# Kernel optimization log

Hardware: AMD Instinct MI355X
Metric: run time of the kernel (lower is better)

The kernel has to match this reference:

```python
import jax, jax.numpy as jnp
import numpy as np

D_MODEL = 1024
NUM_HEADS = 16
D_K = 1024
D_V = 1024
D_IN = 1024
THETA = 10000.0
B, S = 2, 2048


def setup_inputs() -> dict:
    key = jax.random.key(0)
    k1, k2, k3, k4, k5 = jax.random.split(key, 5)
    std_qkv = (2.0 / (D_IN + D_K)) ** 0.5
    std_o = (2.0 / (D_V + D_MODEL)) ** 0.5
    x = jax.random.normal(k1, (B, S, D_IN), jnp.float32)
    wq = jax.random.normal(k2, (D_IN, D_K), jnp.float32) * std_qkv
    wk = jax.random.normal(k3, (D_IN, D_K), jnp.float32) * std_qkv
    wv = jax.random.normal(k4, (D_IN, D_V), jnp.float32) * std_qkv
    wo = jax.random.normal(k5, (D_V, D_MODEL), jnp.float32) * std_o
    return {"x": x, "wq": wq, "wk": wk, "wv": wv, "wo": wo}


def _rope(t, theta):
    # t: (H, B, S, hd) -- interleaved-pair RoPE, angles pos * theta^(-2i/hd)
    hd = t.shape[-1]
    inv_freq = 1.0 / (theta ** (jnp.arange(0, hd, 2, dtype=jnp.float32) / hd))  # (hd/2,)
    pos = jnp.arange(t.shape[-2], dtype=jnp.float32)
    ang = pos[:, None] * inv_freq[None, :]                                       # (S, hd/2)
    cos, sin = jnp.cos(ang), jnp.sin(ang)
    tp = t.reshape(t.shape[:-1] + (hd // 2, 2))
    t0, t1 = tp[..., 0], tp[..., 1]
    out = jnp.stack([t0 * cos - t1 * sin, t0 * sin + t1 * cos], axis=-1)
    return out.reshape(t.shape)


def reference(x, wq, wk, wv, wo):
    b, s, _ = x.shape
    hd = D_K // NUM_HEADS
    hdv = D_V // NUM_HEADS
    # fused QKV proj (math identical to concat-then-matmul)
    q = jnp.einsum('bsd,de->bse', x, wq).reshape(b, s, NUM_HEADS, hd).transpose(2, 0, 1, 3)
    k = jnp.einsum('bsd,de->bse', x, wk).reshape(b, s, NUM_HEADS, hd).transpose(2, 0, 1, 3)
    v = jnp.einsum('bsd,de->bse', x, wv).reshape(b, s, NUM_HEADS, hdv).transpose(2, 0, 1, 3)
    q = _rope(q, THETA)
    k = _rope(k, THETA)
    scale = 1.0 / jnp.sqrt(jnp.asarray(hd, jnp.float32))
    scores = jnp.einsum('hbqd,hbkd->hbqk', q, k) * scale                 # (H,B,S,S)
    causal = jnp.tril(jnp.ones((s, s), dtype=bool))
    scores = jnp.where(causal, scores, -jnp.inf)
    attn = jax.nn.softmax(scores, axis=-1)
    o = jnp.einsum('hbqk,hbkd->hbqd', attn, v)                            # (H,B,S,hdv)
    o = o.transpose(1, 2, 0, 3).reshape(b, s, D_V)                        # merge heads (outer)
    return jnp.einsum('bsd,de->bse', o, wo)
```

## Files before the change

### kernel.cpp

```cpp
#include <hip/hip_runtime.h>
#include <stdint.h>

typedef __attribute__((ext_vector_type(8))) short short8;
typedef __attribute__((ext_vector_type(4))) float f32x4;
typedef __attribute__((ext_vector_type(4))) unsigned short ushort4v;
typedef __attribute__((ext_vector_type(2))) unsigned int uint2v;

static __device__ __forceinline__ unsigned short f2b(float f) {
  union { float f; unsigned int u; } v; v.f = f;
  unsigned int r = v.u + 0x7FFFu + ((v.u >> 16) & 1u);
  return (unsigned short)(r >> 16);
}

static __device__ __forceinline__ float exp2fast(float x) {
#if __has_builtin(__builtin_amdgcn_exp2f)
  return __builtin_amdgcn_exp2f(x);
#else
  return exp2f(x);
#endif
}

static __device__ __forceinline__ unsigned int cvtpk(float lo, float hi) {
  unsigned int r;
  asm("v_cvt_pk_bf16_f32 %0, %1, %2" : "=v"(r) : "v"(lo), "v"(hi));
  return r;
}

static __device__ __forceinline__ float xor16max(float x) {
#if __has_builtin(__builtin_amdgcn_permlane16_swap)
  unsigned u = __float_as_uint(x);
  uint2v r = __builtin_amdgcn_permlane16_swap(u, u, false, false);
  return fmaxf(__uint_as_float(r[0]), __uint_as_float(r[1]));
#else
  return fmaxf(x, __shfl_xor(x, 16));
#endif
}
static __device__ __forceinline__ float xor32max(float x) {
#if __has_builtin(__builtin_amdgcn_permlane32_swap)
  unsigned u = __float_as_uint(x);
  uint2v r = __builtin_amdgcn_permlane32_swap(u, u, false, false);
  return fmaxf(__uint_as_float(r[0]), __uint_as_float(r[1]));
#else
  return fmaxf(x, __shfl_xor(x, 32));
#endif
}
static __device__ __forceinline__ float xor16add(float x) {
#if __has_builtin(__builtin_amdgcn_permlane16_swap)
  unsigned u = __float_as_uint(x);
  uint2v r = __builtin_amdgcn_permlane16_swap(u, u, false, false);
  return __uint_as_float(r[0]) + __uint_as_float(r[1]);
#else
  return x + __shfl_xor(x, 16);
#endif
}
static __device__ __forceinline__ float xor32add(float x) {
#if __has_builtin(__builtin_amdgcn_permlane32_swap)
  unsigned u = __float_as_uint(x);
  uint2v r = __builtin_amdgcn_permlane32_swap(u, u, false, false);
  return __uint_as_float(r[0]) + __uint_as_float(r[1]);
#else
  return x + __shfl_xor(x, 32);
#endif
}

static __device__ __forceinline__ void gload16(const void* g, void* l) {
  __builtin_amdgcn_global_load_lds(
      (const __attribute__((address_space(1))) unsigned int*)g,
      (__attribute__((address_space(3))) unsigned int*)l, 16, 0, 0);
}


__global__ __launch_bounds__(256) void prep_kernel(
    const float* __restrict__ x, const float* __restrict__ wq,
    const float* __restrict__ wk, const float* __restrict__ wv,
    const float* __restrict__ wo, unsigned short* __restrict__ xb,
    unsigned short* __restrict__ wT, float* __restrict__ ct,
    float* __restrict__ st) {
  __shared__ float t[32][33];
  const int bid = blockIdx.x, tid = threadIdx.x;
  if (bid < 4096) {
    int i = (bid * 256 + tid) * 4;
    float4 v = *(const float4*)(x + i);
    ushort4v o = { f2b(v.x), f2b(v.y), f2b(v.z), f2b(v.w) };
    *(ushort4v*)(xb + i) = o;
  } else if (bid < 8192) {
    int tt = bid - 4096;
    int z = tt >> 10, xy = tt & 1023;
    const float* src = (z == 0) ? wq : (z == 1) ? wk : (z == 2) ? wv : wo;
    unsigned short* dst = wT + (size_t)z * 1048576;
    int tx = tid & 31, ty = tid >> 5;
    int n0 = (xy & 31) * 32, k0 = (xy >> 5) * 32;
#pragma unroll
    for (int i = 0; i < 4; ++i) {
      int r = ty + i * 8;
      t[r][tx] = src[(size_t)(k0 + r) * 1024 + n0 + tx];
    }
    __syncthreads();
#pragma unroll
    for (int i = 0; i < 4; ++i) {
      int r = ty + i * 8;
      dst[(size_t)(n0 + r) * 1024 + k0 + tx] = f2b(t[tx][r]);
    }
  } else {
    int i = (bid - 8192) * 256 + tid;
    int s = i >> 5, p = i & 31;
    float ang = (float)s * powf(10000.0f, -(float)(2 * p) / 64.0f);
    ct[i] = cosf(ang);
    st[i] = sinf(ang);
  }
}


__global__ __launch_bounds__(256) void gemm_kernel(
    const unsigned short* __restrict__ A, const unsigned short* __restrict__ WT,
    unsigned short* __restrict__ Qb, unsigned short* __restrict__ Kb,
    unsigned short* __restrict__ VTb,
    const float* __restrict__ ctab, const float* __restrict__ stab) {
  __shared__ unsigned short As[2][128 * 32];
  __shared__ unsigned short Bs[2][128 * 32];
  const int tid = threadIdx.x;
  const int w = tid >> 6, lane = tid & 63;
  const int m0 = blockIdx.x * 128, n0 = blockIdx.y * 128;
  const int mode = blockIdx.z;
  const unsigned short* Bt = WT + (size_t)mode * 1048576;
  const int wr = w >> 1, wc = w & 1;
  const int srow = lane >> 2, scol = lane & 3;
  f32x4 acc[4][4] = {};
  for (int k0 = 0; k0 < 1024; k0 += 64) {
#pragma unroll
    for (int p = 0; p < 2; ++p)
#pragma unroll
      for (int c = 0; c < 2; ++c) {
        int chunk = w * 2 + c;
        gload16(A + (size_t)(m0 + chunk * 16 + srow) * 1024 + k0 + p * 32 + scol * 8,
                (char*)As[p] + chunk * 1024);
        gload16(Bt + (size_t)(n0 + chunk * 16 + srow) * 1024 + k0 + p * 32 + scol * 8,
                (char*)Bs[p] + chunk * 1024);
      }
    __syncthreads();
#pragma unroll
    for (int p = 0; p < 2; ++p) {
      short8 af[4], bf[4];
#pragma unroll
      for (int i = 0; i < 4; ++i) {
        af[i] = *(const short8*)((const char*)As[p] +
                ((wr * 64 + i * 16 + (lane & 15)) * 64 + (lane >> 4) * 16));
        bf[i] = *(const short8*)((const char*)Bs[p] +
                ((wc * 64 + i * 16 + (lane & 15)) * 64 + (lane >> 4) * 16));
      }
#pragma unroll
      for (int i = 0; i < 4; ++i)
#pragma unroll
        for (int j = 0; j < 4; ++j)
          acc[i][j] = __builtin_amdgcn_mfma_f32_16x16x32_bf16(af[i], bf[j], acc[i][j], 0, 0, 0);
    }
    __syncthreads();
  }

  if (mode < 2) {
    unsigned short* dst = mode ? Kb : Qb;
    const float qscale = mode ? 1.0f : 0.125f * 1.44269504088896f;
#pragma unroll
    for (int i = 0; i < 4; ++i) {
#pragma unroll
      for (int j = 0; j < 4; ++j) {
        int n = n0 + wc * 64 + j * 16 + (lane & 15);
        int h = n >> 6, d = n & 63;
        int pairIdx = d >> 1;
        bool even = (n & 1) == 0;
#pragma unroll
        for (int r = 0; r < 4; ++r) {
          int m = m0 + wr * 64 + i * 16 + (lane >> 4) * 4 + r;
          int b = m >> 11, s = m & 2047;
          float v = acc[i][j][r];
          float pv = __shfl_xor(v, 1);
          float c = ctab[s * 32 + pairIdx], sn = stab[s * 32 + pairIdx];
          float ov = (even ? (v * c - pv * sn) : (pv * sn + v * c)) * qscale;
          dst[(size_t)((h * 2 + b) * 2048 + s) * 64 + d] = f2b(ov);
        }
      }
    }
  } else {
#pragma unroll
    for (int i = 0; i < 4; ++i) {
#pragma unroll
      for (int j = 0; j < 4; ++j) {
        int n = n0 + wc * 64 + j * 16 + (lane & 15);
        int h = n >> 6, d = n & 63;
        int mBase = m0 + wr * 64 + i * 16 + (lane >> 4) * 4;
        int b = mBase >> 11, s = mBase & 2047;
        ushort4v pk = { f2b(acc[i][j][0]), f2b(acc[i][j][1]),
                        f2b(acc[i][j][2]), f2b(acc[i][j][3]) };
        *(ushort4v*)(VTb + (size_t)((h * 2 + b) * 64 + d) * 2048 + s) = pk;
      }
    }
  }
}


__global__ __launch_bounds__(128) void gemm_final_kernel(
    const unsigned short* __restrict__ A, const unsigned short* __restrict__ Bt,
    float* __restrict__ Fout) {
  __shared__ unsigned short As[64 * 32];
  __shared__ unsigned short Bs[128 * 32];
  const int tid = threadIdx.x;
  const int w = tid >> 6, lane = tid & 63;
  const int m0 = blockIdx.x * 64, n0 = blockIdx.y * 128;
  const int srow = lane >> 2, scol = lane & 3;
  f32x4 acc[4][4] = {};
  for (int k0 = 0; k0 < 1024; k0 += 32) {
#pragma unroll
    for (int c = 0; c < 2; ++c) {
      int chunk = w * 2 + c;
      gload16(A + (size_t)(m0 + chunk * 16 + srow) * 1024 + k0 + scol * 8,
              (char*)As + chunk * 1024);
    }
#pragma unroll
    for (int c = 0; c < 4; ++c) {
      int chunk = w * 4 + c;
      gload16(Bt + (size_t)(n0 + chunk * 16 + srow) * 1024 + k0 + scol * 8,
              (char*)Bs + chunk * 1024);
    }
    __syncthreads();
    short8 af[4], bf[4];
#pragma unroll
    for (int i = 0; i < 4; ++i) {
      af[i] = *(const short8*)((const char*)As +
              ((i * 16 + (lane & 15)) * 64 + (lane >> 4) * 16));
      bf[i] = *(const short8*)((const char*)Bs +
              ((w * 64 + i * 16 + (lane & 15)) * 64 + (lane >> 4) * 16));
    }
#pragma unroll
    for (int i = 0; i < 4; ++i)
#pragma unroll
      for (int j = 0; j < 4; ++j)
        acc[i][j] = __builtin_amdgcn_mfma_f32_16x16x32_bf16(af[i], bf[j], acc[i][j], 0, 0, 0);
    __syncthreads();
  }
#pragma unroll
  for (int i = 0; i < 4; ++i)
#pragma unroll
    for (int j = 0; j < 4; ++j) {
      int n = n0 + w * 64 + j * 16 + (lane & 15);
#pragma unroll
      for (int r = 0; r < 4; ++r) {
        int m = m0 + i * 16 + (lane >> 4) * 4 + r;
        Fout[(size_t)m * 1024 + n] = acc[i][j][r];
      }
    }
}


__device__ __forceinline__ void proc_tile(
    const short8 aq[2], const unsigned short* Ksb, const unsigned short* Vsb,
    char* Psw, int lq, int lh, int wq16, bool diag,
    float& m, float& ls, f32x4* o) {
  const int swq = (lq & 7) << 4;
  f32x4 sacc[4] = {};
  __builtin_amdgcn_s_setprio(1);
#pragma unroll
  for (int ct = 0; ct < 4; ++ct) {
    const char* base = (const char*)Ksb + (ct * 16 + lq) * 128;
#pragma unroll
    for (int half = 0; half < 2; ++half) {
      short8 ak = *(const short8*)(base + ((half * 64 + lh * 16) ^ swq));
      sacc[ct] = __builtin_amdgcn_mfma_f32_16x16x32_bf16(ak, aq[half], sacc[ct], 0, 0, 0);
    }
  }
  __builtin_amdgcn_s_setprio(0);

  if (diag) {
    int rel = wq16 + lq - 4 * lh;
#pragma unroll
    for (int ct = 0; ct < 4; ++ct)
#pragma unroll
      for (int r = 0; r < 4; ++r)
        if (ct * 16 + r > rel) sacc[ct][r] = -__builtin_inff();
  }

  float mx0 = fmaxf(fmaxf(sacc[0][0], sacc[0][1]), fmaxf(sacc[0][2], sacc[0][3]));
  float mx1 = fmaxf(fmaxf(sacc[1][0], sacc[1][1]), fmaxf(sacc[1][2], sacc[1][3]));
  float mx2 = fmaxf(fmaxf(sacc[2][0], sacc[2][1]), fmaxf(sacc[2][2], sacc[2][3]));
  float mx3 = fmaxf(fmaxf(sacc[3][0], sacc[3][1]), fmaxf(sacc[3][2], sacc[3][3]));
  float mx = fmaxf(fmaxf(mx0, mx1), fmaxf(mx2, mx3));
  mx = xor16max(mx);
  mx = xor32max(mx);
  float nm = fmaxf(m, mx);
  float al = exp2fast(m - nm);
  m = nm;
  float ps = 0.f;
#pragma unroll
  for (int ct = 0; ct < 4; ++ct)
#pragma unroll
    for (int r = 0; r < 4; ++r) {
      float p = exp2fast(sacc[ct][r] - nm);
      sacc[ct][r] = p;
      ps += p;
    }
  ls = ls * al + ps;
#pragma unroll
  for (int ct = 0; ct < 4; ++ct)
#pragma unroll
    for (int r = 0; r < 4; ++r) o[ct][r] *= al;

#pragma unroll
  for (int ct = 0; ct < 4; ++ct) {
    uint2v pk = { cvtpk(sacc[ct][0], sacc[ct][1]), cvtpk(sacc[ct][2], sacc[ct][3]) };
    *(uint2v*)(Psw + lq * 128 + ((ct * 32 + lh * 8) ^ swq)) = pk;
  }
  __builtin_amdgcn_wave_barrier();
  short8 pa[2];
#pragma unroll
  for (int half = 0; half < 2; ++half)
    pa[half] = *(const short8*)(Psw + lq * 128 + ((half * 64 + lh * 16) ^ swq));

  __builtin_amdgcn_s_setprio(1);
#pragma unroll
  for (int ct = 0; ct < 4; ++ct) {
    const char* base = (const char*)Vsb + (ct * 16 + lq) * 128;
#pragma unroll
    for (int half = 0; half < 2; ++half) {
      short8 av = *(const short8*)(base + ((half * 64 + lh * 16) ^ swq));
      o[ct] = __builtin_amdgcn_mfma_f32_16x16x32_bf16(av, pa[half], o[ct], 0, 0, 0);
    }
  }
  __builtin_amdgcn_s_setprio(0);
}

__device__ __forceinline__ void store_o(
    const f32x4* o, float ls, char* Psw, unsigned short* __restrict__ Ob,
    int lane, int lq, int lh, int w, int qb, int h, int b) {
  float l = xor32add(xor16add(ls));
  float invl = 1.0f / l;
#pragma unroll
  for (int ct = 0; ct < 4; ++ct)
#pragma unroll
    for (int r = 0; r < 4; ++r) {
      int d = ct * 16 + lh * 4 + r;
      *(unsigned short*)(Psw + lq * 128 + ((2 * d) ^ ((lq & 7) << 4))) =
          f2b(o[ct][r] * invl);
    }
  __builtin_amdgcn_wave_barrier();
#pragma unroll
  for (int pass = 0; pass < 2; ++pass) {
    int q2 = pass * 8 + (lane >> 3), d0 = (lane & 7) * 8;
    short8 vrow = *(const short8*)(Psw + q2 * 128 + ((2 * d0) ^ ((q2 & 7) << 4)));
    int s = qb + w * 16 + q2;
    *(short8*)(Ob + ((size_t)(b * 2048 + s)) * 1024 + h * 64 + d0) = vrow;
  }
  __builtin_amdgcn_wave_barrier();
}

__global__ __launch_bounds__(256) void attn_kernel(
    const unsigned short* __restrict__ Qb, const unsigned short* __restrict__ Kb,
    const unsigned short* __restrict__ VTb, unsigned short* __restrict__ Ob) {
  __shared__ unsigned short Ks[2][64 * 64];
  __shared__ unsigned short Vs[2][64 * 64];
  __shared__ unsigned short Ps[4 * 16 * 64];
  const int tid = threadIdx.x, w = tid >> 6, lane = tid & 63;
  const int qtL = blockIdx.x, qtH = 31 - blockIdx.x;
  const int hb = blockIdx.y;
  const int h = hb >> 1, b = hb & 1;
  const unsigned short* Qhb = Qb + (size_t)hb * 2048 * 64;
  const unsigned short* Khb = Kb + (size_t)hb * 2048 * 64;
  const unsigned short* Vhb = VTb + (size_t)hb * 64 * 2048;
  char* Psw = (char*)Ps + w * 2048;
  const int lq = lane & 15, lh = lane >> 4;
  const int wq16 = w * 16;

  short8 aqL[2], aqH[2];
  {
    int rowL = qtL * 64 + wq16 + lq;
    int rowH = qtH * 64 + wq16 + lq;
#pragma unroll
    for (int half = 0; half < 2; ++half) {
      aqL[half] = *(const short8*)(Qhb + (size_t)rowL * 64 + half * 32 + lh * 8);
      aqH[half] = *(const short8*)(Qhb + (size_t)rowH * 64 + half * 32 + lh * 8);
    }
  }
  float mL = -__builtin_inff(), lsL = 0.f;
  float mH = -__builtin_inff(), lsH = 0.f;
  f32x4 oL[4] = {}, oH[4] = {};

  const int r0 = tid >> 3, f0 = tid & 7;
  const int so0 = r0 * 128 + ((f0 * 16) ^ ((r0 & 7) << 4));
  short8 gK[2], gV[2];
  gK[0] = *(const short8*)(Khb + (size_t)r0 * 64 + f0 * 8);
  gK[1] = *(const short8*)(Khb + (size_t)(r0 + 32) * 64 + f0 * 8);
  gV[0] = *(const short8*)(Vhb + (size_t)r0 * 2048 + f0 * 8);
  gV[1] = *(const short8*)(Vhb + (size_t)(r0 + 32) * 2048 + f0 * 8);
  *(short8*)((char*)Ks[0] + so0) = gK[0];
  *(short8*)((char*)Ks[0] + so0 + 32 * 128) = gK[1];
  *(short8*)((char*)Vs[0] + so0) = gV[0];
  *(short8*)((char*)Vs[0] + so0 + 32 * 128) = gV[1];
  __syncthreads();

  for (int kt = 0; kt <= qtH; ++kt) {
    const int cur = kt & 1;
    if (kt < qtH) {
      int kk0 = (kt + 1) * 64;
      gK[0] = *(const short8*)(Khb + (size_t)(kk0 + r0) * 64 + f0 * 8);
      gK[1] = *(const short8*)(Khb + (size_t)(kk0 + r0 + 32) * 64 + f0 * 8);
      gV[0] = *(const short8*)(Vhb + (size_t)r0 * 2048 + kk0 + f0 * 8);
      gV[1] = *(const short8*)(Vhb + (size_t)(r0 + 32) * 2048 + kk0 + f0 * 8);
    }
    proc_tile(aqH, Ks[cur], Vs[cur], Psw, lq, lh, wq16, kt == qtH, mH, lsH, oH);
    if (kt <= qtL)
      proc_tile(aqL, Ks[cur], Vs[cur], Psw, lq, lh, wq16, kt == qtL, mL, lsL, oL);
    if (kt < qtH) {
      *(short8*)((char*)Ks[cur ^ 1] + so0) = gK[0];
      *(short8*)((char*)Ks[cur ^ 1] + so0 + 32 * 128) = gK[1];
      *(short8*)((char*)Vs[cur ^ 1] + so0) = gV[0];
      *(short8*)((char*)Vs[cur ^ 1] + so0 + 32 * 128) = gV[1];
    }
    __syncthreads();
  }

  store_o(oL, lsL, Psw, Ob, lane, lq, lh, w, qtL * 64, h, b);
  store_o(oH, lsH, Psw, Ob, lane, lq, lh, w, qtH * 64, h, b);
}


extern "C" void kernel_launch(void* const* d_in, const int* in_sizes, int n_in,
                              void* d_out, int out_size, void* d_ws, size_t ws_size,
                              hipStream_t stream) {
  const float* x  = (const float*)d_in[0];
  const float* wq = (const float*)d_in[1];
  const float* wk = (const float*)d_in[2];
  const float* wv = (const float*)d_in[3];
  const float* wo = (const float*)d_in[4];
  float* out = (float*)d_out;

  char* ws = (char*)d_ws;
  const size_t SZ = 8388608;
  unsigned short* xb  = (unsigned short*)(ws);
  unsigned short* wT  = (unsigned short*)(ws + SZ);
  unsigned short* Qb  = (unsigned short*)(ws + 2 * SZ);
  unsigned short* Kb  = (unsigned short*)(ws + 3 * SZ);
  unsigned short* VTb = (unsigned short*)(ws + 4 * SZ);
  unsigned short* Ob  = (unsigned short*)(ws + 5 * SZ);
  float* ctab = (float*)(ws + 6 * SZ);
  float* stab = (float*)(ws + 6 * SZ + 262144);
  if (ws_size < 6 * SZ + 2 * 262144) return;

  prep_kernel<<<8448, 256, 0, stream>>>(x, wq, wk, wv, wo, xb, wT, ctab, stab);
  gemm_kernel<<<dim3(32, 8, 3), 256, 0, stream>>>(xb, wT, Qb, Kb, VTb, ctab, stab);
  attn_kernel<<<dim3(16, 32), 256, 0, stream>>>(Qb, Kb, VTb, Ob);
  gemm_final_kernel<<<dim3(64, 8), 128, 0, stream>>>(Ob, wT + 3 * 1048576, out);
}
```

Measured before the change: 132.7 us.

## Split attention KV loop by tile parity and merge partials in combine kernel

The attention grid doubles so each block handles only even or odd key tiles for its paired query tiles. Unnormalized partial outputs, row max and row sums go to workspace, and a new combine kernel rescales and merges the two halves into the bf16 output. The aim is more blocks in flight and a shorter per-block serial KV loop on a GPU with many CUs. In exchange it adds an extra launch, partial-output traffic, and reuses xb/Qb/ctab buffers as scratch, which relies on those no longer being needed.

```diff
diff --git a/kernel.cpp b/kernel.cpp
--- a/kernel.cpp
+++ b/kernel.cpp
@@ -327,40 +327,43 @@
   __builtin_amdgcn_s_setprio(0);
 }
 
-__device__ __forceinline__ void store_o(
-    const f32x4* o, float ls, char* Psw, unsigned short* __restrict__ Ob,
-    int lane, int lq, int lh, int w, int qb, int h, int b) {
+__device__ __forceinline__ void store_partial(
+    const f32x4* o, float m, float ls, char* Psw,
+    unsigned short* __restrict__ P, float* __restrict__ mlsT,
+    int lane, int lq, int lh, int w) {
   float l = xor32add(xor16add(ls));
-  float invl = 1.0f / l;
+  if (lh == 0) {
+    mlsT[w * 16 + lq] = m;
+    mlsT[64 + w * 16 + lq] = l;
+  }
 #pragma unroll
   for (int ct = 0; ct < 4; ++ct)
 #pragma unroll
     for (int r = 0; r < 4; ++r) {
       int d = ct * 16 + lh * 4 + r;
-      *(unsigned short*)(Psw + lq * 128 + ((2 * d) ^ ((lq & 7) << 4))) =
-          f2b(o[ct][r] * invl);
+      *(unsigned short*)(Psw + lq * 128 + ((2 * d) ^ ((lq & 7) << 4))) = f2b(o[ct][r]);
     }
   __builtin_amdgcn_wave_barrier();
 #pragma unroll
   for (int pass = 0; pass < 2; ++pass) {
     int q2 = pass * 8 + (lane >> 3), d0 = (lane & 7) * 8;
     short8 vrow = *(const short8*)(Psw + q2 * 128 + ((2 * d0) ^ ((q2 & 7) << 4)));
-    int s = qb + w * 16 + q2;
-    *(short8*)(Ob + ((size_t)(b * 2048 + s)) * 1024 + h * 64 + d0) = vrow;
+    *(short8*)(P + (size_t)(w * 16 + q2) * 64 + d0) = vrow;
   }
   __builtin_amdgcn_wave_barrier();
 }
 
 __global__ __launch_bounds__(256) void attn_kernel(
     const unsigned short* __restrict__ Qb, const unsigned short* __restrict__ Kb,
-    const unsigned short* __restrict__ VTb, unsigned short* __restrict__ Ob) {
+    const unsigned short* __restrict__ VTb, unsigned short* __restrict__ P0,
+    unsigned short* __restrict__ P1, float* __restrict__ mls) {
   __shared__ unsigned short Ks[2][64 * 64];
   __shared__ unsigned short Vs[2][64 * 64];
   __shared__ unsigned short Ps[4 * 16 * 64];
   const int tid = threadIdx.x, w = tid >> 6, lane = tid & 63;
-  const int qtL = blockIdx.x, qtH = 31 - blockIdx.x;
+  const int parity = blockIdx.x >> 4, pi = blockIdx.x & 15;
+  const int qtL = pi, qtH = 31 - pi;
   const int hb = blockIdx.y;
-  const int h = hb >> 1, b = hb & 1;
   const unsigned short* Qhb = Qb + (size_t)hb * 2048 * 64;
   const unsigned short* Khb = Kb + (size_t)hb * 2048 * 64;
   const unsigned short* Vhb = VTb + (size_t)hb * 64 * 2048;
@@ -385,39 +388,80 @@
   const int r0 = tid >> 3, f0 = tid & 7;
   const int so0 = r0 * 128 + ((f0 * 16) ^ ((r0 & 7) << 4));
   short8 gK[2], gV[2];
-  gK[0] = *(const short8*)(Khb + (size_t)r0 * 64 + f0 * 8);
-  gK[1] = *(const short8*)(Khb + (size_t)(r0 + 32) * 64 + f0 * 8);
-  gV[0] = *(const short8*)(Vhb + (size_t)r0 * 2048 + f0 * 8);
-  gV[1] = *(const short8*)(Vhb + (size_t)(r0 + 32) * 2048 + f0 * 8);
+  {
+    int kk0 = parity * 64;
+    gK[0] = *(const short8*)(Khb + (size_t)(kk0 + r0) * 64 + f0 * 8);
+    gK[1] = *(const short8*)(Khb + (size_t)(kk0 + r0 + 32) * 64 + f0 * 8);
+    gV[0] = *(const short8*)(Vhb + (size_t)r0 * 2048 + kk0 + f0 * 8);
+    gV[1] = *(const short8*)(Vhb + (size_t)(r0 + 32) * 2048 + kk0 + f0 * 8);
+  }
   *(short8*)((char*)Ks[0] + so0) = gK[0];
   *(short8*)((char*)Ks[0] + so0 + 32 * 128) = gK[1];
   *(short8*)((char*)Vs[0] + so0) = gV[0];
   *(short8*)((char*)Vs[0] + so0 + 32 * 128) = gV[1];
   __syncthreads();
 
-  for (int kt = 0; kt <= qtH; ++kt) {
-    const int cur = kt & 1;
-    if (kt < qtH) {
-      int kk0 = (kt + 1) * 64;
+  int buf = 0;
+  for (int kt = parity; kt <= qtH; kt += 2) {
+    const bool pf = (kt + 2 <= qtH);
+    if (pf) {
+      int kk0 = (kt + 2) * 64;
       gK[0] = *(const short8*)(Khb + (size_t)(kk0 + r0) * 64 + f0 * 8);
       gK[1] = *(const short8*)(Khb + (size_t)(kk0 + r0 + 32) * 64 + f0 * 8);
       gV[0] = *(const short8*)(Vhb + (size_t)r0 * 2048 + kk0 + f0 * 8);
       gV[1] = *(const short8*)(Vhb + (size_t)(r0 + 32) * 2048 + kk0 + f0 * 8);
     }
-    proc_tile(aqH, Ks[cur], Vs[cur], Psw, lq, lh, wq16, kt == qtH, mH, lsH, oH);
+    proc_tile(aqH, Ks[buf], Vs[buf], Psw, lq, lh, wq16, kt == qtH, mH, lsH, oH);
     if (kt <= qtL)
-      proc_tile(aqL, Ks[cur], Vs[cur], Psw, lq, lh, wq16, kt == qtL, mL, lsL, oL);
-    if (kt < qtH) {
-      *(short8*)((char*)Ks[cur ^ 1] + so0) = gK[0];
-      *(short8*)((char*)Ks[cur ^ 1] + so0 + 32 * 128) = gK[1];
-      *(short8*)((char*)Vs[cur ^ 1] + so0) = gV[0];
-      *(short8*)((char*)Vs[cur ^ 1] + so0 + 32 * 128) = gV[1];
-    }
-    __syncthreads();
-  }
-
-  store_o(oL, lsL, Psw, Ob, lane, lq, lh, w, qtL * 64, h, b);
-  store_o(oH, lsH, Psw, Ob, lane, lq, lh, w, qtH * 64, h, b);
+      proc_tile(aqL, Ks[buf], Vs[buf], Psw, lq, lh, wq16, kt == qtL, mL, lsL, oL);
+    if (pf) {
+      *(short8*)((char*)Ks[buf ^ 1] + so0) = gK[0];
+      *(short8*)((char*)Ks[buf ^ 1] + so0 + 32 * 128) = gK[1];
+      *(short8*)((char*)Vs[buf ^ 1] + so0) = gV[0];
+      *(short8*)((char*)Vs[buf ^ 1] + so0 + 32 * 128) = gV[1];
+    }
+    __syncthreads();
+    buf ^= 1;
+  }
+
+  unsigned short* PP = parity ? P1 : P0;
+  float* mlsP = mls + ((size_t)(parity * 32 + hb) * 32) * 128;
+  store_partial(oL, mL, lsL, Psw, PP + (size_t)(hb * 32 + qtL) * 4096,
+                mlsP + (size_t)qtL * 128, lane, lq, lh, w);
+  store_partial(oH, mH, lsH, Psw, PP + (size_t)(hb * 32 + qtH) * 4096,
+                mlsP + (size_t)qtH * 128, lane, lq, lh, w);
+}
+
+
+__global__ __launch_bounds__(256) void combine_kernel(
+    const unsigned short* __restrict__ P0, const unsigned short* __restrict__ P1,
+    const float* __restrict__ mls, unsigned short* __restrict__ Obf) {
+  const int qt = blockIdx.x, hb = blockIdx.y, t = threadIdx.x;
+  const int q = t >> 2, c0 = (t & 3) * 16;
+  const float* m0p = mls + ((size_t)(0 * 32 + hb) * 32 + qt) * 128;
+  const float* m1p = mls + ((size_t)(1 * 32 + hb) * 32 + qt) * 128;
+  float m0 = m0p[q], ls0 = m0p[64 + q];
+  float m1 = m1p[q], ls1 = m1p[64 + q];
+  float M = fmaxf(m0, m1);
+  float w0 = exp2fast(m0 - M), w1 = exp2fast(m1 - M);
+  float inv = 1.0f / (ls0 * w0 + ls1 * w1);
+  float f0 = w0 * inv, f1 = w1 * inv;
+  size_t base = ((size_t)(hb * 32 + qt) * 64 + q) * 64 + c0;
+  int b = hb & 1, h = hb >> 1;
+  unsigned short* dst = Obf + ((size_t)(b * 2048 + qt * 64 + q)) * 1024 + h * 64 + c0;
+#pragma unroll
+  for (int c = 0; c < 16; c += 8) {
+    union { short8 s; unsigned short u[8]; } a, bb, o;
+    a.s = *(const short8*)(P0 + base + c);
+    bb.s = *(const short8*)(P1 + base + c);
+#pragma unroll
+    for (int e = 0; e < 8; ++e) {
+      float p0 = __uint_as_float((unsigned)a.u[e] << 16);
+      float p1 = __uint_as_float((unsigned)bb.u[e] << 16);
+      o.u[e] = f2b(p0 * f0 + p1 * f1);
+    }
+    *(short8*)(dst + c) = o.s;
+  }
 }
 
 
@@ -438,13 +482,18 @@
   unsigned short* Qb  = (unsigned short*)(ws + 2 * SZ);
   unsigned short* Kb  = (unsigned short*)(ws + 3 * SZ);
   unsigned short* VTb = (unsigned short*)(ws + 4 * SZ);
-  unsigned short* Ob  = (unsigned short*)(ws + 5 * SZ);
+  unsigned short* P0  = (unsigned short*)(ws + 5 * SZ);
   float* ctab = (float*)(ws + 6 * SZ);
-  float* stab = (float*)(ws + 6 * SZ + 262144);
-  if (ws_size < 6 * SZ + 2 * 262144) return;
+  float* stab = ctab + 65536;
+  float* mls  = ctab;
+  if (ws_size < 6 * SZ + 1048576) return;
+
+  unsigned short* P1  = xb;
+  unsigned short* Obf = Qb;
 
   prep_kernel<<<8448, 256, 0, stream>>>(x, wq, wk, wv, wo, xb, wT, ctab, stab);
   gemm_kernel<<<dim3(32, 8, 3), 256, 0, stream>>>(xb, wT, Qb, Kb, VTb, ctab, stab);
-  attn_kernel<<<dim3(16, 32), 256, 0, stream>>>(Qb, Kb, VTb, Ob);
-  gemm_final_kernel<<<dim3(64, 8), 128, 0, stream>>>(Ob, wT + 3 * 1048576, out);
-}
+  attn_kernel<<<dim3(32, 32), 256, 0, stream>>>(Qb, Kb, VTb, P0, P1, mls);
+  combine_kernel<<<dim3(32, 32), 256, 0, stream>>>(P0, P1, mls, Obf);
+  gemm_final_kernel<<<dim3(64, 8), 128, 0, stream>>>(Obf, wT + 3 * 1048576, out);
+}
```

Measured after the change: 140.6 us. 5.9% more time.

## Fuse paired query tiles per K/V tile and defer softmax rescaling

Applied to the files above, without the earlier changes.

The two query tiles (low and high) handled by each block are now processed together for each K/V tile. Each K and V fragment is read from LDS once and fed to MFMAs for both query tiles, which also gives more independent MFMAs to overlap. The online softmax now rescales the running max and output only when some row's new max exceeds the old one by more than 8 (in log2 units), skipping most exp and multiply work. This lazy rescale trades a wave-level vote for the saved work, keeps values bounded by 2^8 in fp32 and bf16 P, and adds register pressure from keeping both score sets live.

```diff
diff --git a/kernel.cpp b/kernel.cpp
--- a/kernel.cpp
+++ b/kernel.cpp
@@ -251,80 +251,56 @@
 }
 
 
-__device__ __forceinline__ void proc_tile(
-    const short8 aq[2], const unsigned short* Ksb, const unsigned short* Vsb,
-    char* Psw, int lq, int lh, int wq16, bool diag,
-    float& m, float& ls, f32x4* o) {
+__device__ __forceinline__ void softmax_defer(f32x4* s, float& m, float& ls, f32x4* o) {
+  float t0 = fmaxf(fmaxf(s[0][0], s[0][1]), fmaxf(s[0][2], s[0][3]));
+  float t1 = fmaxf(fmaxf(s[1][0], s[1][1]), fmaxf(s[1][2], s[1][3]));
+  float t2 = fmaxf(fmaxf(s[2][0], s[2][1]), fmaxf(s[2][2], s[2][3]));
+  float t3 = fmaxf(fmaxf(s[3][0], s[3][1]), fmaxf(s[3][2], s[3][3]));
+  float mx = xor32max(xor16max(fmaxf(fmaxf(t0, t1), fmaxf(t2, t3))));
+  if (__any(mx > m + 8.0f)) {
+    float nm = fmaxf(m, mx);
+    float al = exp2fast(m - nm);
+    m = nm;
+    ls *= al;
+#pragma unroll
+    for (int ct = 0; ct < 4; ++ct)
+#pragma unroll
+      for (int r = 0; r < 4; ++r) o[ct][r] *= al;
+  }
+  float ps0 = 0.f, ps1 = 0.f;
+#pragma unroll
+  for (int ct = 0; ct < 4; ++ct)
+#pragma unroll
+    for (int r = 0; r < 4; ++r) {
+      float p = exp2fast(s[ct][r] - m);
+      s[ct][r] = p;
+      if (ct < 2) ps0 += p; else ps1 += p;
+    }
+  ls += ps0 + ps1;
+}
+
+__device__ __forceinline__ void cmask16(f32x4* s, int rel) {
+#pragma unroll
+  for (int ct = 0; ct < 4; ++ct)
+#pragma unroll
+    for (int r = 0; r < 4; ++r)
+      if (ct * 16 + r > rel) s[ct][r] = -__builtin_inff();
+}
+
+__device__ __forceinline__ void pwrite16(const f32x4* s, char* Psw, int lq, int lh) {
   const int swq = (lq & 7) << 4;
-  f32x4 sacc[4] = {};
-  __builtin_amdgcn_s_setprio(1);
 #pragma unroll
   for (int ct = 0; ct < 4; ++ct) {
-    const char* base = (const char*)Ksb + (ct * 16 + lq) * 128;
-#pragma unroll
-    for (int half = 0; half < 2; ++half) {
-      short8 ak = *(const short8*)(base + ((half * 64 + lh * 16) ^ swq));
-      sacc[ct] = __builtin_amdgcn_mfma_f32_16x16x32_bf16(ak, aq[half], sacc[ct], 0, 0, 0);
-    }
-  }
-  __builtin_amdgcn_s_setprio(0);
-
-  if (diag) {
-    int rel = wq16 + lq - 4 * lh;
-#pragma unroll
-    for (int ct = 0; ct < 4; ++ct)
-#pragma unroll
-      for (int r = 0; r < 4; ++r)
-        if (ct * 16 + r > rel) sacc[ct][r] = -__builtin_inff();
-  }
-
-  float mx0 = fmaxf(fmaxf(sacc[0][0], sacc[0][1]), fmaxf(sacc[0][2], sacc[0][3]));
-  float mx1 = fmaxf(fmaxf(sacc[1][0], sacc[1][1]), fmaxf(sacc[1][2], sacc[1][3]));
-  float mx2 = fmaxf(fmaxf(sacc[2][0], sacc[2][1]), fmaxf(sacc[2][2], sacc[2][3]));
-  float mx3 = fmaxf(fmaxf(sacc[3][0], sacc[3][1]), fmaxf(sacc[3][2], sacc[3][3]));
-  float mx = fmaxf(fmaxf(mx0, mx1), fmaxf(mx2, mx3));
-  mx = xor16max(mx);
-  mx = xor32max(mx);
-  float nm = fmaxf(m, mx);
-  float al = exp2fast(m - nm);
-  m = nm;
-  float ps = 0.f;
-#pragma unroll
-  for (int ct = 0; ct < 4; ++ct)
-#pragma unroll
-    for (int r = 0; r < 4; ++r) {
-      float p = exp2fast(sacc[ct][r] - nm);
-      sacc[ct][r] = p;
-      ps += p;
-    }
-  ls = ls * al + ps;
-#pragma unroll
-  for (int ct = 0; ct < 4; ++ct)
-#pragma unroll
-    for (int r = 0; r < 4; ++r) o[ct][r] *= al;
-
-#pragma unroll
-  for (int ct = 0; ct < 4; ++ct) {
-    uint2v pk = { cvtpk(sacc[ct][0], sacc[ct][1]), cvtpk(sacc[ct][2], sacc[ct][3]) };
+    uint2v pk = { cvtpk(s[ct][0], s[ct][1]), cvtpk(s[ct][2], s[ct][3]) };
     *(uint2v*)(Psw + lq * 128 + ((ct * 32 + lh * 8) ^ swq)) = pk;
   }
-  __builtin_amdgcn_wave_barrier();
-  short8 pa[2];
+}
+
+__device__ __forceinline__ void pread16(short8* pa, const char* Psw, int lq, int lh) {
+  const int swq = (lq & 7) << 4;
 #pragma unroll
   for (int half = 0; half < 2; ++half)
     pa[half] = *(const short8*)(Psw + lq * 128 + ((half * 64 + lh * 16) ^ swq));
-
-  __builtin_amdgcn_s_setprio(1);
-#pragma unroll
-  for (int ct = 0; ct < 4; ++ct) {
-    const char* base = (const char*)Vsb + (ct * 16 + lq) * 128;
-#pragma unroll
-    for (int half = 0; half < 2; ++half) {
-      short8 av = *(const short8*)(base + ((half * 64 + lh * 16) ^ swq));
-      o[ct] = __builtin_amdgcn_mfma_f32_16x16x32_bf16(av, pa[half], o[ct], 0, 0, 0);
-    }
-  }
-  __builtin_amdgcn_s_setprio(0);
 }
 
 __device__ __forceinline__ void store_o(
@@ -367,6 +343,8 @@
   char* Psw = (char*)Ps + w * 2048;
   const int lq = lane & 15, lh = lane >> 4;
   const int wq16 = w * 16;
+  const int swq = (lq & 7) << 4;
+  const int rel = wq16 + lq - 4 * lh;
 
   short8 aqL[2], aqH[2];
   {
@@ -404,9 +382,74 @@
       gV[0] = *(const short8*)(Vhb + (size_t)r0 * 2048 + kk0 + f0 * 8);
       gV[1] = *(const short8*)(Vhb + (size_t)(r0 + 32) * 2048 + kk0 + f0 * 8);
     }
-    proc_tile(aqH, Ks[cur], Vs[cur], Psw, lq, lh, wq16, kt == qtH, mH, lsH, oH);
-    if (kt <= qtL)
-      proc_tile(aqL, Ks[cur], Vs[cur], Psw, lq, lh, wq16, kt == qtL, mL, lsL, oL);
+    const char* Ksb = (const char*)Ks[cur];
+    const char* Vsb = (const char*)Vs[cur];
+    if (kt <= qtL) {
+      f32x4 sH[4] = {}, sL[4] = {};
+      __builtin_amdgcn_s_setprio(1);
+#pragma unroll
+      for (int ct = 0; ct < 4; ++ct) {
+        const char* base = Ksb + (ct * 16 + lq) * 128;
+        short8 ak0 = *(const short8*)(base + ((lh * 16) ^ swq));
+        short8 ak1 = *(const short8*)(base + ((64 + lh * 16) ^ swq));
+        sH[ct] = __builtin_amdgcn_mfma_f32_16x16x32_bf16(ak0, aqH[0], sH[ct], 0, 0, 0);
+        sH[ct] = __builtin_amdgcn_mfma_f32_16x16x32_bf16(ak1, aqH[1], sH[ct], 0, 0, 0);
+        sL[ct] = __builtin_amdgcn_mfma_f32_16x16x32_bf16(ak0, aqL[0], sL[ct], 0, 0, 0);
+        sL[ct] = __builtin_amdgcn_mfma_f32_16x16x32_bf16(ak1, aqL[1], sL[ct], 0, 0, 0);
+      }
+      __builtin_amdgcn_s_setprio(0);
+      if (kt == qtL) cmask16(sL, rel);
+      softmax_defer(sH, mH, lsH, oH);
+      softmax_defer(sL, mL, lsL, oL);
+      short8 paH[2], paL[2];
+      pwrite16(sH, Psw, lq, lh);
+      __builtin_amdgcn_wave_barrier();
+      pread16(paH, Psw, lq, lh);
+      __builtin_amdgcn_wave_barrier();
+      pwrite16(sL, Psw, lq, lh);
+      __builtin_amdgcn_wave_barrier();
+      pread16(paL, Psw, lq, lh);
+      __builtin_amdgcn_s_setprio(1);
+#pragma unroll
+      for (int ct = 0; ct < 4; ++ct) {
+        const char* base = Vsb + (ct * 16 + lq) * 128;
+        short8 av0 = *(const short8*)(base + ((lh * 16) ^ swq));
+        short8 av1 = *(const short8*)(base + ((64 + lh * 16) ^ swq));
+        oH[ct] = __builtin_amdgcn_mfma_f32_16x16x32_bf16(av0, paH[0], oH[ct], 0, 0, 0);
+        oH[ct] = __builtin_amdgcn_mfma_f32_16x16x32_bf16(av1, paH[1], oH[ct], 0, 0, 0);
+        oL[ct] = __builtin_amdgcn_mfma_f32_16x16x32_bf16(av0, paL[0], oL[ct], 0, 0, 0);
+        oL[ct] = __builtin_amdgcn_mfma_f32_16x16x32_bf16(av1, paL[1], oL[ct], 0, 0, 0);
+      }
+      __builtin_amdgcn_s_setprio(0);
+    } else {
+      f32x4 sH[4] = {};
+      __builtin_amdgcn_s_setprio(1);
+#pragma unroll
+      for (int ct = 0; ct < 4; ++ct) {
+        const char* base = Ksb + (ct * 16 + lq) * 128;
+        short8 ak0 = *(const short8*)(base + ((lh * 16) ^ swq));
+        short8 ak1 = *(const short8*)(base + ((64 + lh * 16) ^ swq));
+        sH[ct] = __builtin_amdgcn_mfma_f32_16x16x32_bf16(ak0, aqH[0], sH[ct], 0, 0, 0);
+        sH[ct] = __builtin_amdgcn_mfma_f32_16x16x32_bf16(ak1, aqH[1], sH[ct], 0, 0, 0);
+      }
+      __builtin_amdgcn_s_setprio(0);
+      if (kt == qtH) cmask16(sH, rel);
+      softmax_defer(sH, mH, lsH, oH);
+      short8 paH[2];
+      pwrite16(sH, Psw, lq, lh);
+      __builtin_amdgcn_wave_barrier();
+      pread16(paH, Psw, lq, lh);
+      __builtin_amdgcn_s_setprio(1);
+#pragma unroll
+      for (int ct = 0; ct < 4; ++ct) {
+        const char* base = Vsb + (ct * 16 + lq) * 128;
+        short8 av0 = *(const short8*)(base + ((lh * 16) ^ swq));
+        short8 av1 = *(const short8*)(base + ((64 + lh * 16) ^ swq));
+        oH[ct] = __builtin_amdgcn_mfma_f32_16x16x32_bf16(av0, paH[0], oH[ct], 0, 0, 0);
+        oH[ct] = __builtin_amdgcn_mfma_f32_16x16x32_bf16(av1, paH[1], oH[ct], 0, 0, 0);
+      }
+      __builtin_amdgcn_s_setprio(0);
+    }
     if (kt < qtH) {
       *(short8*)((char*)Ks[cur ^ 1] + so0) = gK[0];
       *(short8*)((char*)Ks[cur ^ 1] + so0 + 32 * 128) = gK[1];
```

Measured after the change: 133.6 us. No clear change (+0.7%).
